# Performance work log

Hardware: AMD Instinct MI355X
Metric: run time of the kernel (lower is better)

Reference implementation:

```python
import jax, jax.numpy as jnp
import numpy as np

N_IN = 512
N_OUT = 256
T = 2048
B = 32


def setup_inputs() -> dict:
    key = jax.random.key(0)
    ks = jax.random.split(key, 9)
    s_in = 1.0 / np.sqrt(N_IN)
    inp = {
        "xt": jax.random.normal(ks[0], (T, B, N_IN), dtype=jnp.float32),
        "ct_forward": jax.random.normal(ks[1], (1, B, N_OUT), dtype=jnp.float32),
        # weights stored torch-style as [out, in]
        "Wx": jax.random.uniform(ks[2], (N_OUT, N_IN), jnp.float32, -s_in, s_in),
        "Wf": jax.random.uniform(ks[3], (N_OUT, N_IN), jnp.float32, -s_in, s_in),
        "bf": jax.random.uniform(ks[4], (N_OUT,), jnp.float32, -s_in, s_in),
        "Wr": jax.random.uniform(ks[5], (N_OUT, N_IN), jnp.float32, -s_in, s_in),
        "br": jax.random.uniform(ks[6], (N_OUT,), jnp.float32, -s_in, s_in),
        "Wc": jax.random.uniform(ks[7], (N_OUT, N_IN), jnp.float32, -s_in, s_in),
        "bc": jax.random.uniform(ks[8], (N_OUT,), jnp.float32, -s_in, s_in),
    }
    return inp


def reference(xt, ct_forward, Wx, Wf, bf, Wr, br, Wc, bc):
    # Batched projections over all timesteps (the GEMM part of SRU).
    x_proj = jnp.einsum("tbi,oi->tbo", xt, Wx)              # [T,B,n_out]
    f = jax.nn.sigmoid(jnp.einsum("tbi,oi->tbo", xt, Wf) + bf)
    r = jax.nn.sigmoid(jnp.einsum("tbi,oi->tbo", xt, Wr) + br)
    cx = jnp.einsum("tbi,oi->tbo", xt, Wc) + bc

    def step(c, inp):
        x_t, ft, rt, cxt = inp
        c = ft * c + (1.0 - ft) * x_t
        h = rt * jnp.tanh(c) + (1.0 - rt) * cxt
        return c, h

    c_final, ht = jax.lax.scan(step, ct_forward[0], (x_proj, f, r, cx))
    # dropout=0.0 -> identity; forward returns (ht, ct)
    return ht, c_final
```

## Files before the change

kernel.cpp:

```cpp
#include <hip/hip_runtime.h>
#include <stdint.h>

#define T_STEPS 2048
#define BATCH   32
#define NIN     512
#define NOUT    256
#define MROWS   (T_STEPS*BATCH)
#define BO      (BATCH*NOUT)
#define NCHUNK  32
#define CHLEN   (T_STEPS/NCHUNK)

typedef _Float16 f16x8 __attribute__((ext_vector_type(8)));
typedef _Float16 f16x4 __attribute__((ext_vector_type(4)));
typedef float    fx4   __attribute__((ext_vector_type(4)));

#define LDSP(p) ((__attribute__((address_space(3))) void*)(p))
#define GLBP(p) ((const __attribute__((address_space(1))) void*)(p))

#define BAR()       asm volatile("s_barrier" ::: "memory")
#define WAITLGKM0() do { asm volatile("s_waitcnt lgkmcnt(0)" ::: "memory"); __builtin_amdgcn_sched_barrier(0); } while(0)
#define WAITVM(n)   do { asm volatile("s_waitcnt vmcnt(" #n ")" ::: "memory"); __builtin_amdgcn_sched_barrier(0); } while(0)

__global__ __launch_bounds__(256) void convert_x(
    const float* __restrict__ xt, _Float16* __restrict__ xh)
{
    long i = ((long)blockIdx.x * 256 + threadIdx.x) * 8;
    float4 v0 = *(const float4*)(xt + i);
    float4 v1 = *(const float4*)(xt + i + 4);
    f16x8 h;
    h[0] = (_Float16)v0.x; h[1] = (_Float16)v0.y;
    h[2] = (_Float16)v0.z; h[3] = (_Float16)v0.w;
    h[4] = (_Float16)v1.x; h[5] = (_Float16)v1.y;
    h[6] = (_Float16)v1.z; h[7] = (_Float16)v1.w;
    *(f16x8*)(xh + i) = h;
}

__global__ __launch_bounds__(256) void convert_w(
    const float* __restrict__ Wx, const float* __restrict__ Wf,
    const float* __restrict__ Wr, const float* __restrict__ Wc,
    _Float16* __restrict__ Wcat)
{
    int idx = blockIdx.x * 256 + threadIdx.x;
    int n  = idx >> 7;
    int k4 = (idx & 127) * 4;
    int g = n >> 8, o = n & 255;
    const float* W = (g == 0) ? Wx : (g == 1) ? Wf : (g == 2) ? Wr : Wc;
    float4 v = *(const float4*)(W + o * NIN + k4);
    f16x4 h;
    h[0] = (_Float16)v.x; h[1] = (_Float16)v.y;
    h[2] = (_Float16)v.z; h[3] = (_Float16)v.w;
    *(f16x4*)(Wcat + n * NIN + k4) = h;
}

#define BM 256
#define BN 256
#define BK 64
#define NGT 32

__global__ __launch_bounds__(512) void gemm_proj(
    const _Float16* __restrict__ xh,
    const _Float16* __restrict__ Wcat,
    const float* __restrict__ bfv, const float* __restrict__ brv, const float* __restrict__ bcv,
    _Float16* __restrict__ xp_h, _Float16* __restrict__ f_h,
    _Float16* __restrict__ r_h,  _Float16* __restrict__ cx_h)
{
    __shared__ char lds[131072];

    const int tid  = threadIdx.x;
    const int lane = tid & 63;
    const int w    = tid >> 6;
    const int wrq  = w >> 2;
    const int wcq  = w & 3;
    const int lr = lane & 15, lk = lane >> 4;

    int wg = (blockIdx.x & 7) * 32 + (blockIdx.x >> 3);
    const int  cg   = wg & 3;
    const int  mgrp = wg >> 2;
    const long m0 = (long)mgrp * 1024;
    const int  n0 = cg * BN;

    const int rl8  = lane >> 3;
    const int scol = (((lane & 7) ^ rl8) << 4);
    const char* baseA = (const char*)xh   + (m0 + w * 8 + rl8) * 1024 + scol;
    const char* baseB = (const char*)Wcat + ((long)(n0 + w * 8 + rl8)) * 1024 + scol;

#define STAGE_A(g, h) do {                                                   \
        char* _d = lds + ((g) & 1) * 32768 + (h) * 16384 + w * 1024;         \
        const char* _s = baseA + (long)((g) >> 3) * 262144                   \
                         + ((g) & 7) * 128 + (long)(h) * 131072;             \
        __builtin_amdgcn_global_load_lds(GLBP(_s),         LDSP(_d),        16, 0, 0); \
        __builtin_amdgcn_global_load_lds(GLBP(_s + 65536), LDSP(_d + 8192), 16, 0, 0); \
    } while (0)
#define STAGE_B(g, h) do {                                                   \
        char* _d = lds + 65536 + ((g) & 1) * 32768 + (h) * 16384 + w * 1024; \
        const char* _s = baseB + ((g) & 7) * 128 + (long)(h) * 131072;       \
        __builtin_amdgcn_global_load_lds(GLBP(_s),         LDSP(_d),        16, 0, 0); \
        __builtin_amdgcn_global_load_lds(GLBP(_s + 65536), LDSP(_d + 8192), 16, 0, 0); \
    } while (0)

    fx4 acc[2][2][4][2];
    #pragma unroll
    for (int a = 0; a < 2; ++a)
        #pragma unroll
        for (int b = 0; b < 2; ++b)
            #pragma unroll
            for (int c = 0; c < 4; ++c)
                #pragma unroll
                for (int d = 0; d < 2; ++d)
                    acc[a][b][c][d] = (fx4){0.f, 0.f, 0.f, 0.f};

    f16x8 Ar[4][2];
    f16x8 B0r[2][2];
    f16x8 B1r[2][2];

#define READ_A(c2, h) do {                                                   \
        _Pragma("unroll")                                                    \
        for (int mf = 0; mf < 4; ++mf) {                                     \
            int rl = wrq * 64 + mf * 16 + lr;                                \
            int rb = (c2) * 32768 + (h) * 16384 + rl * 128;                  \
            _Pragma("unroll")                                                \
            for (int kk = 0; kk < 2; ++kk)                                   \
                Ar[mf][kk] = *(const f16x8*)(lds + rb +                      \
                    ((kk * 64 + lk * 16) ^ ((rl & 7) << 4)));                \
        }                                                                    \
    } while (0)
#define READ_B(c2, h, dst) do {                                              \
        _Pragma("unroll")                                                    \
        for (int nf = 0; nf < 2; ++nf) {                                     \
            int rl = wcq * 32 + nf * 16 + lr;                                \
            int rb = 65536 + (c2) * 32768 + (h) * 16384 + rl * 128;          \
            _Pragma("unroll")                                                \
            for (int kk = 0; kk < 2; ++kk)                                   \
                dst[nf][kk] = *(const f16x8*)(lds + rb +                     \
                    ((kk * 64 + lk * 16) ^ ((rl & 7) << 4)));                \
        }                                                                    \
    } while (0)
#define MMACC(Qr, Qc, Br) do {                                               \
        __builtin_amdgcn_s_setprio(1);                                       \
        _Pragma("unroll")                                                    \
        for (int kk = 0; kk < 2; ++kk)                                       \
            _Pragma("unroll")                                                \
            for (int mf = 0; mf < 4; ++mf)                                   \
                _Pragma("unroll")                                            \
                for (int nf = 0; nf < 2; ++nf)                               \
                    acc[Qr][Qc][mf][nf] = __builtin_amdgcn_mfma_f32_16x16x32_f16( \
                        Br[nf][kk], Ar[mf][kk], acc[Qr][Qc][mf][nf], 0, 0, 0);    \
        __builtin_amdgcn_s_setprio(0);                                       \
    } while (0)

    const int g_out = cg;
    _Float16* outp = (g_out == 0) ? xp_h : (g_out == 1) ? f_h : (g_out == 2) ? r_h : cx_h;
    const float* bias = (g_out == 1) ? bfv : (g_out == 2) ? brv : (g_out == 3) ? bcv : nullptr;

    STAGE_A(0, 0); STAGE_B(0, 0); STAGE_B(0, 1); STAGE_A(0, 1);
    STAGE_A(1, 0); STAGE_B(1, 0);
    WAITVM(4);
    BAR();

    for (int g = 0; g < NGT; ++g) {
        const int c2 = g & 1;
        READ_A(c2, 0);
        READ_B(c2, 0, B0r);
        if (g + 1 < NGT) STAGE_B(g + 1, 1);
        WAITLGKM0();
        MMACC(0, 0, B0r);
        READ_B(c2, 1, B1r);
        if (g + 1 < NGT) STAGE_A(g + 1, 1);
        WAITLGKM0();
        MMACC(0, 1, B1r);
        READ_A(c2, 1);
        BAR();
        if (g + 2 < NGT) STAGE_A(g + 2, 0);
        WAITLGKM0();
        MMACC(1, 0, B0r);
        if (g + 2 < NGT) STAGE_B(g + 2, 0);
        MMACC(1, 1, B1r);
        if (g < NGT - 2)       WAITVM(4);
        else if (g == NGT - 2) WAITVM(0);
        BAR();
        if ((g & 7) == 7) {
            const long mbase = m0 + (long)(g >> 3) * 256;
            #pragma unroll
            for (int Qr = 0; Qr < 2; ++Qr) {
                #pragma unroll
                for (int Qc = 0; Qc < 2; ++Qc) {
                    #pragma unroll
                    for (int nf = 0; nf < 2; ++nf) {
                        const int ob = Qc * 128 + wcq * 32 + nf * 16 + lk * 4;
                        float4 bv4 = (g_out == 0) ? (float4){0.f, 0.f, 0.f, 0.f}
                                                  : *(const float4*)(bias + ob);
                        #pragma unroll
                        for (int mf = 0; mf < 4; ++mf) {
                            long row = mbase + Qr * 128 + wrq * 64 + mf * 16 + lr;
                            fx4 v = acc[Qr][Qc][mf][nf];
                            f16x4 hv;
                            if (g_out == 1 || g_out == 2) {
                                float p0 = v[0] + bv4.x, p1 = v[1] + bv4.y;
                                float p2 = v[2] + bv4.z, p3 = v[3] + bv4.w;
                                hv[0] = (_Float16)(__builtin_amdgcn_rcpf(1.0f + __expf(-p0)));
                                hv[1] = (_Float16)(__builtin_amdgcn_rcpf(1.0f + __expf(-p1)));
                                hv[2] = (_Float16)(__builtin_amdgcn_rcpf(1.0f + __expf(-p2)));
                                hv[3] = (_Float16)(__builtin_amdgcn_rcpf(1.0f + __expf(-p3)));
                            } else {
                                hv[0] = (_Float16)(v[0] + bv4.x);
                                hv[1] = (_Float16)(v[1] + bv4.y);
                                hv[2] = (_Float16)(v[2] + bv4.z);
                                hv[3] = (_Float16)(v[3] + bv4.w);
                            }
                            *(f16x4*)(outp + row * NOUT + ob) = hv;
                            acc[Qr][Qc][mf][nf] = (fx4){0.f, 0.f, 0.f, 0.f};
                        }
                    }
                }
            }
        }
    }
}

__global__ __launch_bounds__(256) void chunk_scan_a(
    const _Float16* __restrict__ f_h, const _Float16* __restrict__ xp_h,
    float* __restrict__ chunkA, float* __restrict__ chunkB)
{
    int tid2 = blockIdx.x * 256 + threadIdx.x;
    int ch = tid2 >> 11;
    int b4 = (tid2 & 2047) << 2;
    long base = (long)ch * CHLEN * BO + b4;
    fx4 a = (fx4){1.f, 1.f, 1.f, 1.f};
    fx4 cc = (fx4){0.f, 0.f, 0.f, 0.f};
    for (int s = 0; s < CHLEN; ++s) {
        long i = base + (long)s * BO;
        f16x4 fv = *(const f16x4*)(f_h + i);
        f16x4 xv = *(const f16x4*)(xp_h + i);
        #pragma unroll
        for (int q = 0; q < 4; ++q) {
            float f = (float)fv[q], x = (float)xv[q];
            cc[q] = f * cc[q] + (1.f - f) * x;
            a[q] *= f;
        }
    }
    *(fx4*)(chunkA + ch * BO + b4) = a;
    *(fx4*)(chunkB + ch * BO + b4) = cc;
}

__global__ __launch_bounds__(256) void chunk_prop(
    const float* __restrict__ ct0,
    const float* __restrict__ chunkA, const float* __restrict__ chunkB,
    float* __restrict__ cin, float* __restrict__ c_final)
{
    int bo = blockIdx.x * 256 + threadIdx.x;
    float c = ct0[bo];
    #pragma unroll
    for (int ch = 0; ch < NCHUNK; ++ch) {
        cin[ch * BO + bo] = c;
        c = chunkA[ch * BO + bo] * c + chunkB[ch * BO + bo];
    }
    c_final[bo] = c;
}

__global__ __launch_bounds__(256) void chunk_scan_h(
    const _Float16* __restrict__ xp_h, const _Float16* __restrict__ f_h,
    const _Float16* __restrict__ r_h,  const _Float16* __restrict__ cx_h,
    const float* __restrict__ cin, float* __restrict__ ht)
{
    int tid2 = blockIdx.x * 256 + threadIdx.x;
    int ch = tid2 >> 11;
    int b4 = (tid2 & 2047) << 2;
    long base = (long)ch * CHLEN * BO + b4;
    fx4 c = *(const fx4*)(cin + ch * BO + b4);
    for (int s = 0; s < CHLEN; ++s) {
        long i = base + (long)s * BO;
        f16x4 fv  = *(const f16x4*)(f_h + i);
        f16x4 xv  = *(const f16x4*)(xp_h + i);
        f16x4 rv  = *(const f16x4*)(r_h + i);
        f16x4 cxv = *(const f16x4*)(cx_h + i);
        fx4 h4;
        #pragma unroll
        for (int q = 0; q < 4; ++q) {
            float f = (float)fv[q], x = (float)xv[q];
            float r = (float)rv[q], cx = (float)cxv[q];
            c[q] = f * c[q] + (1.f - f) * x;
            float e = __expf(2.f * c[q]);
            float th = (e - 1.f) * __builtin_amdgcn_rcpf(e + 1.f);
            h4[q] = r * th + (1.f - r) * cx;
        }
        *(fx4*)(ht + i) = h4;
    }
}

extern "C" void kernel_launch(void* const* d_in, const int* in_sizes, int n_in,
                              void* d_out, int out_size, void* d_ws, size_t ws_size,
                              hipStream_t stream) {
    const float* xt  = (const float*)d_in[0];
    const float* ct0 = (const float*)d_in[1];
    const float* Wx  = (const float*)d_in[2];
    const float* Wf  = (const float*)d_in[3];
    const float* bf_ = (const float*)d_in[4];
    const float* Wr  = (const float*)d_in[5];
    const float* br_ = (const float*)d_in[6];
    const float* Wc  = (const float*)d_in[7];
    const float* bc_ = (const float*)d_in[8];

    float* ht      = (float*)d_out;
    float* c_final = ht + (size_t)MROWS * NOUT;

    char* ws = (char*)d_ws;
    _Float16* Wcat = (_Float16*)ws;
    _Float16* xh   = (_Float16*)(ws + (1 << 20));
    _Float16* xp_h = xh + (size_t)MROWS * NIN;
    _Float16* f_h  = xp_h + (size_t)MROWS * NOUT;
    _Float16* r_h  = f_h  + (size_t)MROWS * NOUT;
    _Float16* cx_h = r_h  + (size_t)MROWS * NOUT;
    float* chunkA  = (float*)(cx_h + (size_t)MROWS * NOUT);
    float* chunkB  = chunkA + NCHUNK * BO;
    float* cin     = chunkB + NCHUNK * BO;

    convert_w<<<512, 256, 0, stream>>>(Wx, Wf, Wr, Wc, Wcat);
    convert_x<<<(MROWS * NIN / 8) / 256, 256, 0, stream>>>(xt, xh);
    gemm_proj<<<256, 512, 0, stream>>>(
        xh, Wcat, bf_, br_, bc_, xp_h, f_h, r_h, cx_h);
    chunk_scan_a<<<256, 256, 0, stream>>>(f_h, xp_h, chunkA, chunkB);
    chunk_prop<<<BO / 256, 256, 0, stream>>>(ct0, chunkA, chunkB, cin, c_final);
    chunk_scan_h<<<256, 256, 0, stream>>>(xp_h, f_h, r_h, cx_h, cin, ht);
}
```

Before: 194.7 us.

## Fuse fp32-to-fp16 conversion of x into GEMM A-tile staging

Drops the separate convert_x kernel. The GEMM now loads fp32 x straight from global memory into registers, converts it to fp16 and writes it into swizzled LDS, replacing the async global_load_lds path for A. This removes a full pass that wrote and re-read the 64 MB fp16 copy of x (128 MB fp32 read) plus one kernel launch. In exchange the GEMM reads twice the A bytes, spends VGPRs on staging registers, and replaces direct-to-LDS loads with register round trips, and its waitcnt and barrier schedule is reworked.

```diff
diff --git a/kernel.cpp b/kernel.cpp
--- a/kernel.cpp
+++ b/kernel.cpp
@@ -17,23 +17,9 @@
 #define LDSP(p) ((__attribute__((address_space(3))) void*)(p))
 #define GLBP(p) ((const __attribute__((address_space(1))) void*)(p))
 
-#define BAR()       asm volatile("s_barrier" ::: "memory")
-#define WAITLGKM0() do { asm volatile("s_waitcnt lgkmcnt(0)" ::: "memory"); __builtin_amdgcn_sched_barrier(0); } while(0)
-#define WAITVM(n)   do { asm volatile("s_waitcnt vmcnt(" #n ")" ::: "memory"); __builtin_amdgcn_sched_barrier(0); } while(0)
-
-__global__ __launch_bounds__(256) void convert_x(
-    const float* __restrict__ xt, _Float16* __restrict__ xh)
-{
-    long i = ((long)blockIdx.x * 256 + threadIdx.x) * 8;
-    float4 v0 = *(const float4*)(xt + i);
-    float4 v1 = *(const float4*)(xt + i + 4);
-    f16x8 h;
-    h[0] = (_Float16)v0.x; h[1] = (_Float16)v0.y;
-    h[2] = (_Float16)v0.z; h[3] = (_Float16)v0.w;
-    h[4] = (_Float16)v1.x; h[5] = (_Float16)v1.y;
-    h[6] = (_Float16)v1.z; h[7] = (_Float16)v1.w;
-    *(f16x8*)(xh + i) = h;
-}
+#define BAR()        asm volatile("s_barrier" ::: "memory")
+#define WAITLGKM0()  do { asm volatile("s_waitcnt lgkmcnt(0)" ::: "memory"); __builtin_amdgcn_sched_barrier(0); } while(0)
+#define WAITVM(n)    do { asm volatile("s_waitcnt vmcnt(" #n ")" ::: "memory"); __builtin_amdgcn_sched_barrier(0); } while(0)
 
 __global__ __launch_bounds__(256) void convert_w(
     const float* __restrict__ Wx, const float* __restrict__ Wf,
@@ -58,7 +44,7 @@
 #define NGT 32
 
 __global__ __launch_bounds__(512) void gemm_proj(
-    const _Float16* __restrict__ xh,
+    const float*    __restrict__ xt,
     const _Float16* __restrict__ Wcat,
     const float* __restrict__ bfv, const float* __restrict__ brv, const float* __restrict__ bcv,
     _Float16* __restrict__ xp_h, _Float16* __restrict__ f_h,
@@ -79,17 +65,30 @@
     const long m0 = (long)mgrp * 1024;
     const int  n0 = cg * BN;
 
+    const char* baseAg = (const char*)xt + (m0 + (tid >> 4)) * 2048 + (tid & 15) * 16;
+    const int awbase = (tid >> 4) * 128 + (((tid & 15) * 8) ^ (((tid >> 4) & 7) << 4));
+
     const int rl8  = lane >> 3;
     const int scol = (((lane & 7) ^ rl8) << 4);
-    const char* baseA = (const char*)xh   + (m0 + w * 8 + rl8) * 1024 + scol;
     const char* baseB = (const char*)Wcat + ((long)(n0 + w * 8 + rl8)) * 1024 + scol;
 
-#define STAGE_A(g, h) do {                                                   \
-        char* _d = lds + ((g) & 1) * 32768 + (h) * 16384 + w * 1024;         \
-        const char* _s = baseA + (long)((g) >> 3) * 262144                   \
-                         + ((g) & 7) * 128 + (long)(h) * 131072;             \
-        __builtin_amdgcn_global_load_lds(GLBP(_s),         LDSP(_d),        16, 0, 0); \
-        __builtin_amdgcn_global_load_lds(GLBP(_s + 65536), LDSP(_d + 8192), 16, 0, 0); \
+    float4 av0[4], av1[4];
+#define ALOAD_H(gi, half, dst) do {                                          \
+        const char* _b = baseAg + (long)((gi) >> 3) * 524288                 \
+                         + ((gi) & 7) * 256 + (half) * 262144;               \
+        _Pragma("unroll")                                                    \
+        for (int jj = 0; jj < 4; ++jj)                                       \
+            dst[jj] = *(const float4*)(_b + jj * 65536);                     \
+    } while (0)
+#define AWRITE_H(gi, half, src) do {                                         \
+        char* _d = lds + ((gi) & 1) * 32768 + (half) * 16384 + awbase;       \
+        _Pragma("unroll")                                                    \
+        for (int jj = 0; jj < 4; ++jj) {                                     \
+            f16x4 _h;                                                        \
+            _h[0] = (_Float16)src[jj].x; _h[1] = (_Float16)src[jj].y;        \
+            _h[2] = (_Float16)src[jj].z; _h[3] = (_Float16)src[jj].w;        \
+            *(f16x4*)(_d + jj * 4096) = _h;                                  \
+        }                                                                    \
     } while (0)
 #define STAGE_B(g, h) do {                                                   \
         char* _d = lds + 65536 + ((g) & 1) * 32768 + (h) * 16384 + w * 1024; \
@@ -152,31 +151,38 @@
     _Float16* outp = (g_out == 0) ? xp_h : (g_out == 1) ? f_h : (g_out == 2) ? r_h : cx_h;
     const float* bias = (g_out == 1) ? bfv : (g_out == 2) ? brv : (g_out == 3) ? bcv : nullptr;
 
-    STAGE_A(0, 0); STAGE_B(0, 0); STAGE_B(0, 1); STAGE_A(0, 1);
-    STAGE_A(1, 0); STAGE_B(1, 0);
-    WAITVM(4);
+    ALOAD_H(0, 0, av0); ALOAD_H(0, 1, av1);
+    STAGE_B(0, 0); STAGE_B(0, 1); STAGE_B(1, 0);
+    WAITVM(6);
+    AWRITE_H(0, 0, av0); AWRITE_H(0, 1, av1);
+    ALOAD_H(1, 0, av0);
+    WAITVM(6);
+    WAITLGKM0();
     BAR();
 
     for (int g = 0; g < NGT; ++g) {
         const int c2 = g & 1;
         READ_A(c2, 0);
         READ_B(c2, 0, B0r);
+        if (g >= 1 && g + 1 < NGT) ALOAD_H(g + 1, 0, av0);
         if (g + 1 < NGT) STAGE_B(g + 1, 1);
         WAITLGKM0();
         MMACC(0, 0, B0r);
         READ_B(c2, 1, B1r);
-        if (g + 1 < NGT) STAGE_A(g + 1, 1);
+        if (g + 1 < NGT) ALOAD_H(g + 1, 1, av1);
         WAITLGKM0();
         MMACC(0, 1, B1r);
         READ_A(c2, 1);
+        if (g < NGT - 1) { WAITVM(6); } else { WAITVM(0); }
+        if (g + 1 < NGT) AWRITE_H(g + 1, 0, av0);
         BAR();
-        if (g + 2 < NGT) STAGE_A(g + 2, 0);
         WAITLGKM0();
         MMACC(1, 0, B0r);
         if (g + 2 < NGT) STAGE_B(g + 2, 0);
+        if (g < NGT - 2) { WAITVM(2); } else { WAITVM(0); }
+        if (g + 1 < NGT) AWRITE_H(g + 1, 1, av1);
         MMACC(1, 1, B1r);
-        if (g < NGT - 2)       WAITVM(4);
-        else if (g == NGT - 2) WAITVM(0);
+        WAITLGKM0();
         BAR();
         if ((g & 7) == 7) {
             const long mbase = m0 + (long)(g >> 3) * 256;
@@ -305,8 +311,7 @@
 
     char* ws = (char*)d_ws;
     _Float16* Wcat = (_Float16*)ws;
-    _Float16* xh   = (_Float16*)(ws + (1 << 20));
-    _Float16* xp_h = xh + (size_t)MROWS * NIN;
+    _Float16* xp_h = (_Float16*)(ws + (1 << 20));
     _Float16* f_h  = xp_h + (size_t)MROWS * NOUT;
     _Float16* r_h  = f_h  + (size_t)MROWS * NOUT;
     _Float16* cx_h = r_h  + (size_t)MROWS * NOUT;
@@ -315,9 +320,8 @@
     float* cin     = chunkB + NCHUNK * BO;
 
     convert_w<<<512, 256, 0, stream>>>(Wx, Wf, Wr, Wc, Wcat);
-    convert_x<<<(MROWS * NIN / 8) / 256, 256, 0, stream>>>(xt, xh);
     gemm_proj<<<256, 512, 0, stream>>>(
-        xh, Wcat, bf_, br_, bc_, xp_h, f_h, r_h, cx_h);
+        xt, Wcat, bf_, br_, bc_, xp_h, f_h, r_h, cx_h);
     chunk_scan_a<<<256, 256, 0, stream>>>(f_h, xp_h, chunkA, chunkB);
     chunk_prop<<<BO / 256, 256, 0, stream>>>(ct0, chunkA, chunkB, cin, c_final);
     chunk_scan_h<<<256, 256, 0, stream>>>(xp_h, f_h, r_h, cx_h, cin, ht);
```

New measurement: 195.1 us. No clear change (+0.2%).
